# Kernel optimization log

Measured on AMD Instinct MI355X. Metric: run time of the kernel, lower is better.

Reference implementation:

```python
import jax, jax.numpy as jnp
import numpy as np

EPS = 1e-5      # InstanceNorm2d default eps
SLOPE = 0.2     # leaky relu negative_slope
K = 16          # neighbors
C = 128         # feature_dim


def _knn_idx(coords, k):
    # coords: [B,3,N] -> idx [B,N,k] of k nearest neighbors (excluding self)
    x = jnp.transpose(coords, (0, 2, 1))            # [B,N,3]
    sq = jnp.sum(x * x, axis=-1)                    # [B,N]
    dist = sq[:, :, None] + sq[:, None, :] - 2.0 * jnp.einsum('bnd,bmd->bnm', x, x)
    _, idx = jax.lax.top_k(-dist, k + 1)            # smallest distances, sorted
    return idx[:, :, 1:]                            # drop self


def _graph_feature(feats, idx):
    # feats: [B,C,N], idx: [B,N,k] -> [B,2C,N,k] = cat(center, neighbor-center)
    neigh = jax.vmap(lambda f, i: f[:, i])(feats, idx)   # [B,C,N,k]
    center = feats[:, :, :, None]
    return jnp.concatenate(
        [jnp.broadcast_to(center, neigh.shape), neigh - center], axis=1)


def _inorm(x):
    # InstanceNorm2d (affine=False): normalize each (b,c) over spatial dims
    mean = jnp.mean(x, axis=(2, 3), keepdims=True)
    var = jnp.mean((x - mean) ** 2, axis=(2, 3), keepdims=True)
    return (x - mean) * jax.lax.rsqrt(var + EPS)


def _edge_block(x, W):
    # 1x1 conv (W: [O,I]) + instance norm + leaky relu, x: [B,I,N,k]
    h = jnp.einsum('oi,bink->bonk', W, x)
    return jax.nn.leaky_relu(_inorm(h), SLOPE)


def setup_inputs() -> dict:
    key = jax.random.key(0)
    k1, k2, k3, k4, k5 = jax.random.split(key, 5)
    B, N = 2, 8192
    coords = jax.random.normal(k1, (B, 3, N), dtype=jnp.float32)
    features = jax.random.normal(k2, (B, C, N), dtype=jnp.float32)
    W1 = jax.random.normal(k3, (C, 2 * C), dtype=jnp.float32) * 0.05
    W2 = jax.random.normal(k4, (2 * C, 2 * C), dtype=jnp.float32) * 0.05
    W3 = jax.random.normal(k5, (C, 4 * C), dtype=jnp.float32) * 0.05
    return {"coords": coords, "features": features, "W1": W1, "W2": W2, "W3": W3}


def reference(coords, features, W1, W2, W3):
    idx = _knn_idx(coords, K)                       # [B,N,K]
    x0 = features                                   # [B,C,N]
    # block 1: EdgeConv C -> C
    x1 = _edge_block(_graph_feature(x0, idx), W1)   # [B,C,N,K]
    x1 = jnp.max(x1, axis=-1)                       # [B,C,N]
    # block 2: EdgeConv C -> 2C (same coords => same knn indices)
    x2 = _edge_block(_graph_feature(x1, idx), W2)   # [B,2C,N,K]
    x2 = jnp.max(x2, axis=-1)                       # [B,2C,N]
    # fuse: 1x1 conv 4C -> C + instance norm (over N) + leaky relu
    x3 = jnp.concatenate([x0, x1, x2], axis=1)      # [B,4C,N]
    h = jnp.einsum('oi,bin->bon', W3, x3)           # [B,C,N]
    h = _inorm(h[:, :, :, None])[:, :, :, 0]
    return jax.nn.leaky_relu(h, SLOPE)
```

## Files before the change

### kernel.cpp

```cpp
#include <hip/hip_runtime.h>
#include <hip/hip_bf16.h>
#include <cstdint>
#include <cstddef>

#define B_ 2
#define N_ 8192
#define C_ 128
#define K_ 16
#define NK_ (N_ * K_)
#define EPS_ 1e-5f
#define SLOPE_ 0.2f
#define INF_ 3.0e38f

typedef __attribute__((ext_vector_type(8))) short short8;
typedef __attribute__((ext_vector_type(4))) float f32x4;

static constexpr size_t OFF_IDX   = 0x000000;
static constexpr size_t OFF_CPK   = 0x100000;
static constexpr size_t OFF_CPK64 = 0x140000;
static constexpr size_t OFF_ACC   = 0x1C0000;
static constexpr size_t OFF_WC1   = 0x1D0000;
static constexpr size_t OFF_WC2   = 0x1E0000;
static constexpr size_t OFF_WB3   = 0x200000;
static constexpr size_t OFF_X3T   = 0x240000;
static constexpr size_t OFF_PQ    = OFF_X3T + (size_t)B_ * N_ * 512 * 2;

__device__ __forceinline__ __hip_bfloat16 ftob(float f) { return __float2bfloat16(f); }
__device__ __forceinline__ float bf2f(unsigned short h) {
  unsigned u = ((unsigned)h) << 16;
  return __uint_as_float(u);
}

__global__ void prep_kernel(const float* __restrict__ coords,
                            const float* __restrict__ W1,
                            const float* __restrict__ W2,
                            const float* __restrict__ W3,
                            __hip_bfloat16* __restrict__ wc1, __hip_bfloat16* __restrict__ wc2,
                            __hip_bfloat16* __restrict__ wb3,
                            float4* __restrict__ cpk, double4* __restrict__ cpk64,
                            float* __restrict__ acc) {
  int tid = blockIdx.x * 256 + threadIdx.x;
  if (tid < 32768) {
    int o = tid >> 7, i = tid & 127;
    float v;
    if (o < 128) v = W1[o * 256 + i] - W1[o * 256 + 128 + i];
    else         v = W1[(o - 128) * 256 + 128 + i];
    wc1[tid] = ftob(v);
  } else if (tid < 32768 + 65536) {
    int t2 = tid - 32768;
    int o = t2 >> 7, i = t2 & 127;
    float v;
    if (o < 256) v = W2[o * 256 + i] - W2[o * 256 + 128 + i];
    else         v = W2[(o - 256) * 256 + 128 + i];
    wc2[t2] = ftob(v);
  } else if (tid < 98304 + 65536) {
    int t2 = tid - 98304;
    wb3[t2] = ftob(W3[t2]);
  } else if (tid < 163840 + B_ * N_) {
    int q = tid - 163840;
    int b = q >> 13, n = q & (N_ - 1);
    float x = coords[(b * 3 + 0) * N_ + n];
    float y = coords[(b * 3 + 1) * N_ + n];
    float z = coords[(b * 3 + 2) * N_ + n];
    float sq = __fadd_rn(__fadd_rn(__fmul_rn(x, x), __fmul_rn(y, y)), __fmul_rn(z, z));
    cpk[q] = make_float4(x, y, z, sq);
    double xd = (double)x, yd = (double)y, zd = (double)z;
    double sqd = (xd * xd + yd * yd) + zd * zd;
    cpk64[q] = make_double4(xd, yd, zd, sqd);
  } else if (tid < 180224 + 2048) {
    acc[tid - 180224] = 0.f;
  }
}

__global__ __launch_bounds__(256) void transpose_kernel(const float* __restrict__ x0,
                                                        __hip_bfloat16* __restrict__ x3t) {
  __shared__ float tile[64 * 68];
  int b = blockIdx.z, c0 = blockIdx.y * 64, n0 = blockIdx.x * 64;
  int t = threadIdx.x;
  int r = t >> 4;
  int c4 = (t & 15) * 4;
#pragma unroll
  for (int i = 0; i < 4; ++i) {
    int row = r + i * 16;
    float4 v = *(const float4*)&x0[((size_t)(b * C_ + c0 + row)) * N_ + n0 + c4];
    *(float4*)&tile[row * 68 + c4] = v;
  }
  __syncthreads();
#pragma unroll
  for (int i = 0; i < 4; ++i) {
    int nl = r + i * 16;
    __hip_bfloat16* dst = &x3t[((size_t)(b * N_ + n0 + nl)) * 512 + c0 + c4];
    dst[0] = ftob(tile[(c4 + 0) * 68 + nl]);
    dst[1] = ftob(tile[(c4 + 1) * 68 + nl]);
    dst[2] = ftob(tile[(c4 + 2) * 68 + nl]);
    dst[3] = ftob(tile[(c4 + 3) * 68 + nl]);
  }
}

__device__ __forceinline__ float thresh17(float v, int lane) {
#pragma unroll
  for (int k2 = 2; k2 <= 64; k2 <<= 1) {
#pragma unroll
    for (int j = k2 >> 1; j > 0; j >>= 1) {
      float o = __shfl_xor(v, j, 64);
      bool up = ((lane & k2) == 0);
      bool lower = ((lane & j) == 0);
      v = ((lower == up)) ? fminf(v, o) : fmaxf(v, o);
    }
  }
  return __shfl(v, 16, 64);
}

__device__ __forceinline__ void bsort64d(double& d, int& ix, int lane) {
#pragma unroll
  for (int k2 = 2; k2 <= 64; k2 <<= 1) {
#pragma unroll
    for (int j = k2 >> 1; j > 0; j >>= 1) {
      double od = __shfl_xor(d, j, 64);
      int oi = __shfl_xor(ix, j, 64);
      bool up = ((lane & k2) == 0);
      bool lower = ((lane & j) == 0);
      bool takeMin = (lower == up);
      bool less = (od < d) || (od == d && oi < ix);
      if (takeMin == less) { d = od; ix = oi; }
    }
  }
}

__global__ __launch_bounds__(256) void knn_kernel(const float4* __restrict__ cpk,
                                                  const double4* __restrict__ cpk64,
                                                  int* __restrict__ idxout) {
  __shared__ int scnt[4][4];
  __shared__ int sii[4][4][128];
  int lane = threadIdx.x & 63;
  int wv = threadIdx.x >> 6;
  int q0 = (blockIdx.x * 4 + wv) * 4;
  int b = q0 >> 13;
  const float4* cb = cpk + (size_t)b * N_;
  const double4* cb64 = cpk64 + (size_t)b * N_;
  float4 me0 = cpk[q0], me1 = cpk[q0 + 1], me2 = cpk[q0 + 2], me3 = cpk[q0 + 3];
  float a0x = -2.f * me0.x, a0y = -2.f * me0.y, a0z = -2.f * me0.z;
  float a1x = -2.f * me1.x, a1y = -2.f * me1.y, a1z = -2.f * me1.z;
  float a2x = -2.f * me2.x, a2y = -2.f * me2.y, a2z = -2.f * me2.z;
  float a3x = -2.f * me3.x, a3y = -2.f * me3.y, a3z = -2.f * me3.z;

  if (lane < 4) scnt[wv][lane] = 0;
  __syncthreads();

  float m0 = INF_, m1 = INF_, m2 = INF_, m3 = INF_;
  for (int i = 0; i < 128; ++i) {
    float4 c = cb[i * 64 + lane];
    m0 = fminf(m0, fmaf(a0z, c.z, fmaf(a0y, c.y, fmaf(a0x, c.x, c.w))));
    m1 = fminf(m1, fmaf(a1z, c.z, fmaf(a1y, c.y, fmaf(a1x, c.x, c.w))));
    m2 = fminf(m2, fmaf(a2z, c.z, fmaf(a2y, c.y, fmaf(a2x, c.x, c.w))));
    m3 = fminf(m3, fmaf(a3z, c.z, fmaf(a3y, c.y, fmaf(a3x, c.x, c.w))));
  }
  float T0 = thresh17(m0, lane) + 1e-3f;
  float T1 = thresh17(m1, lane) + 1e-3f;
  float T2 = thresh17(m2, lane) + 1e-3f;
  float T3 = thresh17(m3, lane) + 1e-3f;

  for (int i = 0; i < 128; ++i) {
    float4 c = cb[i * 64 + lane];
    float p0 = fmaf(a0z, c.z, fmaf(a0y, c.y, fmaf(a0x, c.x, c.w)));
    float p1 = fmaf(a1z, c.z, fmaf(a1y, c.y, fmaf(a1x, c.x, c.w)));
    float p2 = fmaf(a2z, c.z, fmaf(a2y, c.y, fmaf(a2x, c.x, c.w)));
    float p3 = fmaf(a3z, c.z, fmaf(a3y, c.y, fmaf(a3x, c.x, c.w)));
    bool h0 = p0 <= T0, h1 = p1 <= T1, h2 = p2 <= T2, h3 = p3 <= T3;
    if (h0 | h1 | h2 | h3) {
      int m = i * 64 + lane;
      if (h0) { int p = atomicAdd(&scnt[wv][0], 1); if (p < 128) sii[wv][0][p] = m; }
      if (h1) { int p = atomicAdd(&scnt[wv][1], 1); if (p < 128) sii[wv][1][p] = m; }
      if (h2) { int p = atomicAdd(&scnt[wv][2], 1); if (p < 128) sii[wv][2][p] = m; }
      if (h3) { int p = atomicAdd(&scnt[wv][3], 1); if (p < 128) sii[wv][3][p] = m; }
    }
  }
  __syncthreads();

#pragma unroll 1
  for (int j = 0; j < 4; ++j) {
    int q = q0 + j;
    int n = q & (N_ - 1);
    int cnt = scnt[wv][j] < 128 ? scnt[wv][j] : 128;
    double4 me64 = cb64[n];
    double d1 = 1e300; int ix1 = 0x7FFFFFFF;
    if (lane < cnt) {
      int m = sii[wv][j][lane];
      if (m != n) {
        double4 c = cb64[m];
        double dot = (me64.x * c.x + me64.y * c.y) + me64.z * c.z;
        d1 = (me64.w + c.w) - 2.0 * dot;
        ix1 = m;
      }
    }
    bsort64d(d1, ix1, lane);
    if (cnt > 64) {
      double d2 = 1e300; int ix2 = 0x7FFFFFFF;
      if (lane + 64 < cnt) {
        int m = sii[wv][j][lane + 64];
        if (m != n) {
          double4 c = cb64[m];
          double dot = (me64.x * c.x + me64.y * c.y) + me64.z * c.z;
          d2 = (me64.w + c.w) - 2.0 * dot;
          ix2 = m;
        }
      }
      bsort64d(d2, ix2, lane);
      int src = (lane - 16) & 63;
      double dB = __shfl(d2, src, 64);
      int iB = __shfl(ix2, src, 64);
      double nd = (lane < 16) ? d1 : ((lane < 32) ? dB : 1e300);
      int nix = (lane < 16) ? ix1 : ((lane < 32) ? iB : 0x7FFFFFFF);
      bsort64d(nd, nix, lane);
      d1 = nd; ix1 = nix;
    }
    if (lane < 16) idxout[(size_t)q * 16 + lane] = ix1;
  }
}

template <typename OUT>
__global__ __launch_bounds__(256) void gemm_mfma(const __hip_bfloat16* __restrict__ X, int ldx,
                                                 const __hip_bfloat16* __restrict__ W, int ldw,
                                                 OUT* __restrict__ Cc, int ldc, int Ktot) {
  __shared__ short As[64 * 40];
  int b = blockIdx.z;
  int n0 = blockIdx.x * 64, o0 = blockIdx.y * 64;
  int t = threadIdx.x;
  int lane = t & 63, wv = t >> 6;
  int nh = (wv & 1) * 32, oh = (wv >> 1) * 32;
  const __hip_bfloat16* Xb = X + (size_t)(b * N_ + n0) * ldx;
  f32x4 acc00 = {0.f, 0.f, 0.f, 0.f}, acc01 = acc00, acc10 = acc00, acc11 = acc00;
  int sr = t >> 2;
  int sc = (t & 3) * 8;
  int arow = lane & 15;
  int kq = (lane >> 4) * 8;
  for (int kt = 0; kt < Ktot; kt += 32) {
    short8 av = *(const short8*)&Xb[(size_t)sr * ldx + kt + sc];
    *(short8*)&As[sr * 40 + sc] = av;
    __syncthreads();
    short8 a0 = *(const short8*)&As[(nh + arow) * 40 + kq];
    short8 a1 = *(const short8*)&As[(nh + 16 + arow) * 40 + kq];
    const __hip_bfloat16* Wp = W + (size_t)(o0 + oh + arow) * ldw + kt + kq;
    short8 b0 = *(const short8*)&Wp[0];
    short8 b1 = *(const short8*)&Wp[16 * (size_t)ldw];
    acc00 = __builtin_amdgcn_mfma_f32_16x16x32_bf16(a0, b0, acc00, 0, 0, 0);
    acc01 = __builtin_amdgcn_mfma_f32_16x16x32_bf16(a0, b1, acc01, 0, 0, 0);
    acc10 = __builtin_amdgcn_mfma_f32_16x16x32_bf16(a1, b0, acc10, 0, 0, 0);
    acc11 = __builtin_amdgcn_mfma_f32_16x16x32_bf16(a1, b1, acc11, 0, 0, 0);
    __syncthreads();
  }
  int crow = (lane >> 4) * 4;
  int ccol = lane & 15;
#pragma unroll
  for (int r = 0; r < 4; ++r) {
    size_t row0 = (size_t)(b * N_ + n0 + nh + crow + r) * ldc + o0 + oh;
    size_t row1 = (size_t)(b * N_ + n0 + nh + 16 + crow + r) * ldc + o0 + oh;
    if constexpr (sizeof(OUT) == 4) {
      Cc[row0 + ccol]      = acc00[r];
      Cc[row0 + 16 + ccol] = acc01[r];
      Cc[row1 + ccol]      = acc10[r];
      Cc[row1 + 16 + ccol] = acc11[r];
    } else {
      Cc[row0 + ccol]      = ftob(acc00[r]);
      Cc[row0 + 16 + ccol] = ftob(acc01[r]);
      Cc[row1 + ccol]      = ftob(acc10[r]);
      Cc[row1 + 16 + ccol] = ftob(acc11[r]);
    }
  }
}

template <int CO>
__global__ __launch_bounds__(256) void edge_kernel(const __hip_bfloat16* __restrict__ PQ,
                                                   const int* __restrict__ idx,
                                                   __hip_bfloat16* __restrict__ Mout,
                                                   float* __restrict__ acc) {
  constexpr int CP = CO / 2;
  constexpr int NG = 256 / CP;
  __shared__ float r1a[256], r1b[256], r2a[256], r2b[256];
  int b = blockIdx.y;
  int n0 = blockIdx.x * 64;
  int t = threadIdx.x;
  int oc = t & (CP - 1);
  int o2 = oc * 2;
  int qg = t / CP;
  float s1a = 0.f, s1b = 0.f, s2a = 0.f, s2b = 0.f;
  const __hip_bfloat16* PQb = PQ + (size_t)b * N_ * (2 * CO);
  for (int qq = qg; qq < 64; qq += NG) {
    int n = n0 + qq;
    const int4* ip = (const int4*)&idx[(size_t)(b * N_ + n) * 16];
    int4 i0 = ip[0], i1 = ip[1], i2 = ip[2], i3 = ip[3];
    unsigned pu = *(const unsigned*)&PQb[(size_t)n * (2 * CO) + o2];
    float pa = bf2f((unsigned short)(pu & 0xFFFF));
    float pb = bf2f((unsigned short)(pu >> 16));
    float hma = -INF_, hmb = -INF_;
#define EDGE_STEP(mm)                                                         \
    { int mc = (mm) & (N_ - 1);                                               \
      unsigned vu = *(const unsigned*)&PQb[(size_t)mc * (2 * CO) + CO + o2];  \
      float ha = pa + bf2f((unsigned short)(vu & 0xFFFF));                    \
      float hb = pb + bf2f((unsigned short)(vu >> 16));                       \
      hma = fmaxf(hma, ha); s1a += ha; s2a = fmaf(ha, ha, s2a);               \
      hmb = fmaxf(hmb, hb); s1b += hb; s2b = fmaf(hb, hb, s2b); }
    EDGE_STEP(i0.x) EDGE_STEP(i0.y) EDGE_STEP(i0.z) EDGE_STEP(i0.w)
    EDGE_STEP(i1.x) EDGE_STEP(i1.y) EDGE_STEP(i1.z) EDGE_STEP(i1.w)
    EDGE_STEP(i2.x) EDGE_STEP(i2.y) EDGE_STEP(i2.z) EDGE_STEP(i2.w)
    EDGE_STEP(i3.x) EDGE_STEP(i3.y) EDGE_STEP(i3.z) EDGE_STEP(i3.w)
#undef EDGE_STEP
    __hip_bfloat162 hh;
    hh.x = ftob(hma); hh.y = ftob(hmb);
    *(__hip_bfloat162*)&Mout[(size_t)(b * N_ + n) * 512 + o2] = hh;
  }
  r1a[t] = s1a; r1b[t] = s1b; r2a[t] = s2a; r2b[t] = s2b;
  __syncthreads();
  if (t < CP) {
#pragma unroll
    for (int g = 1; g < NG; ++g) {
      s1a += r1a[t + g * CP]; s1b += r1b[t + g * CP];
      s2a += r2a[t + g * CP]; s2b += r2b[t + g * CP];
    }
    atomicAdd(&acc[(b * CO + o2) * 2 + 0], s1a);
    atomicAdd(&acc[(b * CO + o2) * 2 + 1], s2a);
    atomicAdd(&acc[(b * CO + o2 + 1) * 2 + 0], s1b);
    atomicAdd(&acc[(b * CO + o2 + 1) * 2 + 1], s2b);
  }
}

template <int CO>
__global__ void norm_kernel(__hip_bfloat16* __restrict__ M, const float* __restrict__ acc) {
  int tid = blockIdx.x * 256 + threadIdx.x;
  int o = tid & (CO - 1);
  int bn = tid / CO;
  int b = bn >> 13;
  float s1 = acc[(b * CO + o) * 2], s2 = acc[(b * CO + o) * 2 + 1];
  const float inv = 1.f / (float)NK_;
  float mean = s1 * inv;
  float var = fmaf(s2, inv, -mean * mean);
  float rs = rsqrtf(var + EPS_);
  float v = __bfloat162float(M[(size_t)bn * 512 + o]);
  float y = (v - mean) * rs;
  M[(size_t)bn * 512 + o] = ftob(y > 0.f ? y : SLOPE_ * y);
}

__global__ __launch_bounds__(256) void colred_kernel(const float* __restrict__ H,
                                                     float* __restrict__ acc3) {
  __shared__ float r1[256], r2[256];
  int b = blockIdx.y;
  int n0 = blockIdx.x * 256;
  int t = threadIdx.x;
  int o = t & 127, half = t >> 7;
  float s1 = 0.f, s2 = 0.f;
  for (int i = 0; i < 128; ++i) {
    int n = n0 + half * 128 + i;
    float v = H[(size_t)(b * N_ + n) * 128 + o];
    s1 += v; s2 = fmaf(v, v, s2);
  }
  r1[t] = s1; r2[t] = s2;
  __syncthreads();
  if (t < 128) {
    s1 = r1[t] + r1[t + 128];
    s2 = r2[t] + r2[t + 128];
    atomicAdd(&acc3[(b * 128 + o) * 2 + 0], s1);
    atomicAdd(&acc3[(b * 128 + o) * 2 + 1], s2);
  }
}

__global__ __launch_bounds__(256) void final_kernel(const float* __restrict__ H,
                                                    const float* __restrict__ acc3,
                                                    float* __restrict__ out) {
  __shared__ float tile[64 * 132];
  int b = blockIdx.y, n0 = blockIdx.x * 64;
  int t = threadIdx.x;
  int r = t >> 5;
  int c4 = (t & 31) * 4;
#pragma unroll
  for (int i = 0; i < 8; ++i) {
    int row = r + i * 8;
    *(float4*)&tile[row * 132 + c4] = *(const float4*)&H[(size_t)(b * N_ + n0 + row) * 128 + c4];
  }
  __syncthreads();
  int o = t >> 1;
  int nh = (t & 1) * 32;
  float s1 = acc3[(b * 128 + o) * 2], s2 = acc3[(b * 128 + o) * 2 + 1];
  const float inv = 1.f / (float)N_;
  float mean = s1 * inv;
  float var = fmaf(s2, inv, -mean * mean);
  float rs = rsqrtf(var + EPS_);
#pragma unroll
  for (int i = 0; i < 32; ++i) {
    int nl = nh + i;
    float v = tile[nl * 132 + o];
    float y = (v - mean) * rs;
    y = y > 0.f ? y : SLOPE_ * y;
    out[(size_t)(b * 128 + o) * N_ + n0 + nl] = y;
  }
}

extern "C" void kernel_launch(void* const* d_in, const int* in_sizes, int n_in,
                              void* d_out, int out_size, void* d_ws, size_t ws_size,
                              hipStream_t stream) {
  const float* coords = (const float*)d_in[0];
  const float* feats = (const float*)d_in[1];
  const float* W1 = (const float*)d_in[2];
  const float* W2 = (const float*)d_in[3];
  const float* W3 = (const float*)d_in[4];
  char* ws = (char*)d_ws;
  int* idx = (int*)(ws + OFF_IDX);
  float4* cpk = (float4*)(ws + OFF_CPK);
  double4* cpk64 = (double4*)(ws + OFF_CPK64);
  float* acc = (float*)(ws + OFF_ACC);
  __hip_bfloat16* wc1 = (__hip_bfloat16*)(ws + OFF_WC1);
  __hip_bfloat16* wc2 = (__hip_bfloat16*)(ws + OFF_WC2);
  __hip_bfloat16* wb3 = (__hip_bfloat16*)(ws + OFF_WB3);
  __hip_bfloat16* x3t = (__hip_bfloat16*)(ws + OFF_X3T);
  __hip_bfloat16* pqb = (__hip_bfloat16*)(ws + OFF_PQ);
  float* ht = (float*)(ws + OFF_PQ);

  prep_kernel<<<712, 256, 0, stream>>>(coords, W1, W2, W3, wc1, wc2, wb3, cpk, cpk64, acc);
  transpose_kernel<<<dim3(128, 2, 2), 256, 0, stream>>>(feats, x3t);
  knn_kernel<<<1024, 256, 0, stream>>>(cpk, cpk64, idx);
  gemm_mfma<__hip_bfloat16><<<dim3(128, 4, 2), 256, 0, stream>>>(x3t, 512, wc1, 128, pqb, 256, 128);
  edge_kernel<128><<<dim3(128, 2), 256, 0, stream>>>(pqb, idx, x3t + 128, acc + 0);
  norm_kernel<128><<<(B_ * N_ * 128) / 256, 256, 0, stream>>>(x3t + 128, acc + 0);
  gemm_mfma<__hip_bfloat16><<<dim3(128, 8, 2), 256, 0, stream>>>(x3t + 128, 512, wc2, 128, pqb, 512, 128);
  edge_kernel<256><<<dim3(128, 2), 256, 0, stream>>>(pqb, idx, x3t + 256, acc + 512);
  norm_kernel<256><<<(B_ * N_ * 256) / 256, 256, 0, stream>>>(x3t + 256, acc + 512);
  gemm_mfma<float><<<dim3(128, 2, 2), 256, 0, stream>>>(x3t, 512, wb3, 512, ht, 128, 512);
  colred_kernel<<<dim3(32, 2), 256, 0, stream>>>(ht, acc + 1536);
  final_kernel<<<dim3(128, 2), 256, 0, stream>>>(ht, acc + 1536, (float*)d_out);
}
```

Before: 211.2 us.

## Fuse instance-norm into GEMM loads and raise grid parallelism of edge/reduction kernels

Removes the two standalone norm kernels. The instance-norm plus leaky-relu is now applied on the fly as bf16 X tiles are loaded into shared memory in the following GEMMs, with mean and rstd recomputed from the accumulated sums. Edge, column-reduction and final kernels get smaller per-block work and 4-8x more blocks to fill the GPU. The trade-off is redundant norm math in every GEMM block and more atomics in the reductions.

```diff
diff --git a/kernel.cpp b/kernel.cpp
--- a/kernel.cpp
+++ b/kernel.cpp
@@ -29,6 +29,10 @@
 __device__ __forceinline__ float bf2f(unsigned short h) {
   unsigned u = ((unsigned)h) << 16;
   return __uint_as_float(u);
+}
+__device__ __forceinline__ short f2bs(float f) {
+  __hip_bfloat16 h = __float2bfloat16(f);
+  return *reinterpret_cast<short*>(&h);
 }
 
 __global__ void prep_kernel(const float* __restrict__ coords,
@@ -218,10 +222,11 @@
   }
 }
 
-template <typename OUT>
+template <typename OUT, int NORM>
 __global__ __launch_bounds__(256) void gemm_mfma(const __hip_bfloat16* __restrict__ X, int ldx,
                                                  const __hip_bfloat16* __restrict__ W, int ldw,
-                                                 OUT* __restrict__ Cc, int ldc, int Ktot) {
+                                                 OUT* __restrict__ Cc, int ldc, int Ktot,
+                                                 const float* __restrict__ nacc) {
   __shared__ short As[64 * 40];
   int b = blockIdx.z;
   int n0 = blockIdx.x * 64, o0 = blockIdx.y * 64;
@@ -236,6 +241,32 @@
   int kq = (lane >> 4) * 8;
   for (int kt = 0; kt < Ktot; kt += 32) {
     short8 av = *(const short8*)&Xb[(size_t)sr * ldx + kt + sc];
+    if constexpr (NORM != 0) {
+      int k = kt + sc;
+      const float* pa = nullptr;
+      if constexpr (NORM == 2) {
+        if (k >= 128 && k < 256) pa = nacc + ((size_t)b * 128 + (k - 128)) * 2;
+        else if (k >= 256)       pa = nacc + 512 + ((size_t)b * 256 + (k - 256)) * 2;
+      } else {
+        pa = nacc + ((size_t)b * 128 + k) * 2;
+      }
+      if (pa) {
+        const float inv = 1.f / (float)NK_;
+        short8 outv;
+#pragma unroll
+        for (int j = 0; j < 8; ++j) {
+          float s1 = pa[2 * j], s2 = pa[2 * j + 1];
+          float mean = s1 * inv;
+          float var = fmaf(s2, inv, -mean * mean);
+          float rs = rsqrtf(var + EPS_);
+          float v = bf2f((unsigned short)av[j]);
+          float y = (v - mean) * rs;
+          y = y > 0.f ? y : SLOPE_ * y;
+          outv[j] = f2bs(y);
+        }
+        av = outv;
+      }
+    }
     *(short8*)&As[sr * 40 + sc] = av;
     __syncthreads();
     short8 a0 = *(const short8*)&As[(nh + arow) * 40 + kq];
@@ -278,14 +309,14 @@
   constexpr int NG = 256 / CP;
   __shared__ float r1a[256], r1b[256], r2a[256], r2b[256];
   int b = blockIdx.y;
-  int n0 = blockIdx.x * 64;
+  int n0 = blockIdx.x * 16;
   int t = threadIdx.x;
   int oc = t & (CP - 1);
   int o2 = oc * 2;
   int qg = t / CP;
   float s1a = 0.f, s1b = 0.f, s2a = 0.f, s2b = 0.f;
   const __hip_bfloat16* PQb = PQ + (size_t)b * N_ * (2 * CO);
-  for (int qq = qg; qq < 64; qq += NG) {
+  for (int qq = qg; qq < 16; qq += NG) {
     int n = n0 + qq;
     const int4* ip = (const int4*)&idx[(size_t)(b * N_ + n) * 16];
     int4 i0 = ip[0], i1 = ip[1], i2 = ip[2], i3 = ip[3];
@@ -324,32 +355,16 @@
   }
 }
 
-template <int CO>
-__global__ void norm_kernel(__hip_bfloat16* __restrict__ M, const float* __restrict__ acc) {
-  int tid = blockIdx.x * 256 + threadIdx.x;
-  int o = tid & (CO - 1);
-  int bn = tid / CO;
-  int b = bn >> 13;
-  float s1 = acc[(b * CO + o) * 2], s2 = acc[(b * CO + o) * 2 + 1];
-  const float inv = 1.f / (float)NK_;
-  float mean = s1 * inv;
-  float var = fmaf(s2, inv, -mean * mean);
-  float rs = rsqrtf(var + EPS_);
-  float v = __bfloat162float(M[(size_t)bn * 512 + o]);
-  float y = (v - mean) * rs;
-  M[(size_t)bn * 512 + o] = ftob(y > 0.f ? y : SLOPE_ * y);
-}
-
 __global__ __launch_bounds__(256) void colred_kernel(const float* __restrict__ H,
                                                      float* __restrict__ acc3) {
   __shared__ float r1[256], r2[256];
   int b = blockIdx.y;
-  int n0 = blockIdx.x * 256;
+  int n0 = blockIdx.x * 32;
   int t = threadIdx.x;
   int o = t & 127, half = t >> 7;
   float s1 = 0.f, s2 = 0.f;
-  for (int i = 0; i < 128; ++i) {
-    int n = n0 + half * 128 + i;
+  for (int i = 0; i < 16; ++i) {
+    int n = n0 + half * 16 + i;
     float v = H[(size_t)(b * N_ + n) * 128 + o];
     s1 += v; s2 = fmaf(v, v, s2);
   }
@@ -366,26 +381,26 @@
 __global__ __launch_bounds__(256) void final_kernel(const float* __restrict__ H,
                                                     const float* __restrict__ acc3,
                                                     float* __restrict__ out) {
-  __shared__ float tile[64 * 132];
-  int b = blockIdx.y, n0 = blockIdx.x * 64;
+  __shared__ float tile[32 * 132];
+  int b = blockIdx.y, n0 = blockIdx.x * 32;
   int t = threadIdx.x;
-  int r = t >> 5;
-  int c4 = (t & 31) * 4;
-#pragma unroll
-  for (int i = 0; i < 8; ++i) {
-    int row = r + i * 8;
-    *(float4*)&tile[row * 132 + c4] = *(const float4*)&H[(size_t)(b * N_ + n0 + row) * 128 + c4];
+  int r = t >> 3;
+  int c8 = t & 7;
+#pragma unroll
+  for (int i = 0; i < 4; ++i) {
+    int col4 = (c8 + i * 8) * 4;
+    *(float4*)&tile[r * 132 + col4] = *(const float4*)&H[(size_t)(b * N_ + n0 + r) * 128 + col4];
   }
   __syncthreads();
   int o = t >> 1;
-  int nh = (t & 1) * 32;
+  int nh = (t & 1) * 16;
   float s1 = acc3[(b * 128 + o) * 2], s2 = acc3[(b * 128 + o) * 2 + 1];
   const float inv = 1.f / (float)N_;
   float mean = s1 * inv;
   float var = fmaf(s2, inv, -mean * mean);
   float rs = rsqrtf(var + EPS_);
 #pragma unroll
-  for (int i = 0; i < 32; ++i) {
+  for (int i = 0; i < 16; ++i) {
     int nl = nh + i;
     float v = tile[nl * 132 + o];
     float y = (v - mean) * rs;
@@ -417,13 +432,11 @@
   prep_kernel<<<712, 256, 0, stream>>>(coords, W1, W2, W3, wc1, wc2, wb3, cpk, cpk64, acc);
   transpose_kernel<<<dim3(128, 2, 2), 256, 0, stream>>>(feats, x3t);
   knn_kernel<<<1024, 256, 0, stream>>>(cpk, cpk64, idx);
-  gemm_mfma<__hip_bfloat16><<<dim3(128, 4, 2), 256, 0, stream>>>(x3t, 512, wc1, 128, pqb, 256, 128);
-  edge_kernel<128><<<dim3(128, 2), 256, 0, stream>>>(pqb, idx, x3t + 128, acc + 0);
-  norm_kernel<128><<<(B_ * N_ * 128) / 256, 256, 0, stream>>>(x3t + 128, acc + 0);
-  gemm_mfma<__hip_bfloat16><<<dim3(128, 8, 2), 256, 0, stream>>>(x3t + 128, 512, wc2, 128, pqb, 512, 128);
-  edge_kernel<256><<<dim3(128, 2), 256, 0, stream>>>(pqb, idx, x3t + 256, acc + 512);
-  norm_kernel<256><<<(B_ * N_ * 256) / 256, 256, 0, stream>>>(x3t + 256, acc + 512);
-  gemm_mfma<float><<<dim3(128, 2, 2), 256, 0, stream>>>(x3t, 512, wb3, 512, ht, 128, 512);
-  colred_kernel<<<dim3(32, 2), 256, 0, stream>>>(ht, acc + 1536);
-  final_kernel<<<dim3(128, 2), 256, 0, stream>>>(ht, acc + 1536, (float*)d_out);
-}
+  gemm_mfma<__hip_bfloat16, 0><<<dim3(128, 4, 2), 256, 0, stream>>>(x3t, 512, wc1, 128, pqb, 256, 128, nullptr);
+  edge_kernel<128><<<dim3(512, 2), 256, 0, stream>>>(pqb, idx, x3t + 128, acc + 0);
+  gemm_mfma<__hip_bfloat16, 1><<<dim3(128, 8, 2), 256, 0, stream>>>(x3t + 128, 512, wc2, 128, pqb, 512, 128, acc);
+  edge_kernel<256><<<dim3(512, 2), 256, 0, stream>>>(pqb, idx, x3t + 256, acc + 512);
+  gemm_mfma<float, 2><<<dim3(128, 2, 2), 256, 0, stream>>>(x3t, 512, wb3, 512, ht, 128, 512, acc);
+  colred_kernel<<<dim3(256, 2), 256, 0, stream>>>(ht, acc + 1536);
+  final_kernel<<<dim3(256, 2), 256, 0, stream>>>(ht, acc + 1536, (float*)d_out);
+}
```

Measured after the change: 309.1 us. 1.46x slower.
